# Kernel optimization log

Measured on AMD Instinct MI355X. Metric: run time of the kernel, lower is better.

## Reference

```python
import jax, jax.numpy as jnp
import numpy as np
from jax import lax

# --- static config (matches init_kwargs) ---
K_NAT, P_NAT, NHEAD, DM, L = 5, 2, 8, 128, 3
PK, OV, STRIDE = 4, 2, 2          # patcher kernel / overlap / stride = PK-OV
PPAD = PK - OV                    # circular pad for patcher/depatcher crop
RK, RC = 5, 12                    # res layer kernel, hidden channels = 3*4
DN = ('NCHW', 'OIHW', 'NCHW')


def setup_inputs() -> dict:
    key = jax.random.key(0)
    ks = jax.random.split(key, 16)
    B, C, H, W = 2, 3, 256, 256
    rn = lambda k, shape, s=0.02: jax.random.normal(k, shape, jnp.float32) * s
    return {
        'x': jax.random.normal(ks[0], (B, C, H, W), jnp.float32),
        'pos_w': jax.random.uniform(ks[1], (C, H, W), jnp.float32) + 0.5,
        'pos_b': jax.random.uniform(ks[2], (C, H, W), jnp.float32) - 0.5,
        'patch_w': rn(ks[3], (DM, C, PK, PK), 0.05),
        'patch_b': jnp.zeros((DM,), jnp.float32),
        'ln1_g': jnp.ones((L, DM), jnp.float32),
        'ln1_b': jnp.zeros((L, DM), jnp.float32),
        'qkv_w': rn(ks[4], (L, 3 * DM, DM)),
        'qkv_b': jnp.zeros((L, 3 * DM), jnp.float32),
        'rpb': rn(ks[5], (L, NHEAD, 2 * K_NAT - 1, 2 * K_NAT - 1)),
        'proj_w': rn(ks[6], (L, DM, DM)),
        'proj_b': jnp.zeros((L, DM), jnp.float32),
        'ln2_g': jnp.ones((L, DM), jnp.float32),
        'ln2_b': jnp.zeros((L, DM), jnp.float32),
        'fc1_w': rn(ks[7], (L, 4 * DM, DM)),
        'fc1_b': jnp.zeros((L, 4 * DM), jnp.float32),
        'fc2_w': rn(ks[8], (L, DM, 4 * DM)),
        'fc2_b': jnp.zeros((L, DM), jnp.float32),
        'depatch_w': rn(ks[9], (DM, C, PK, PK), 0.05),   # ConvTranspose2d weight (Cin,Cout,kh,kw)
        'depatch_b': jnp.zeros((C,), jnp.float32),
        'res_cv1_w': rn(ks[10], (RC, C, RK, RK), 0.05),
        'res_cv1_b': jnp.zeros((RC,), jnp.float32),
        'res_cv2_w': rn(ks[11], (C, RC, 1, 1), 0.05),
        'res_cv2_b': jnp.zeros((C,), jnp.float32),
    }


def _layer_norm(x, g, b):
    m = x.mean(-1, keepdims=True)
    v = x.var(-1, keepdims=True)
    return (x - m) * lax.rsqrt(v + 1e-5) * g + b


def _nat_block(x, ln1_g, ln1_b, qkv_w, qkv_b, rpb, proj_w, proj_b,
               ln2_g, ln2_b, fc1_w, fc1_b, fc2_w, fc2_b):
    # x: (B,H,W,C). NATLayer: LN -> circular pad by k//2 -> NA -> crop -> residual -> LN -> MLP -> residual.
    # After padding, every kept (interior) pixel has a full centered kxk neighborhood,
    # so we compute q only at interior positions and gather kxk K/V windows from the padded map.
    B, H, W, C = x.shape
    k, p, h = K_NAT, P_NAT, NHEAD
    dh = C // h
    y = _layer_norm(x, ln1_g, ln1_b)
    y = jnp.pad(y, ((0, 0), (p, p), (p, p), (0, 0)), mode='wrap')  # circular
    qkv = y @ qkv_w.T + qkv_b                                      # (B,H+2p,W+2p,3C)
    q, kk, vv = jnp.split(qkv, 3, axis=-1)
    q = q[:, p:p + H, p:p + W].reshape(B, H, W, h, dh) * (dh ** -0.5)
    def win(t):
        t = t.reshape(B, H + 2 * p, W + 2 * p, h, dh)
        return jnp.stack([t[:, i:i + H, j:j + W]
                          for i in range(k) for j in range(k)], axis=3)  # (B,H,W,k*k,h,dh)
    kw, vw = win(kk), win(vv)
    bias = rpb[:, p:p + k, p:p + k].reshape(h, k * k)  # centered slice of (2k-1,2k-1) RPB
    logits = jnp.einsum('bxyhd,bxynhd->bxyhn', q, kw) + bias
    a = jax.nn.softmax(logits, axis=-1)
    o = jnp.einsum('bxyhn,bxynhd->bxyhd', a, vw).reshape(B, H, W, C)
    x = x + (o @ proj_w.T + proj_b)
    y = _layer_norm(x, ln2_g, ln2_b)
    y = jax.nn.leaky_relu(y @ fc1_w.T + fc1_b) @ fc2_w.T + fc2_b
    return x + y


def _forward(x, pos_w, pos_b, patch_w, patch_b, ln1_g, ln1_b, qkv_w, qkv_b,
             rpb, proj_w, proj_b, ln2_g, ln2_b, fc1_w, fc1_b, fc2_w, fc2_b,
             depatch_w, depatch_b, res_cv1_w, res_cv1_b, res_cv2_w, res_cv2_b):
    # positional embedding (dropout is identity, p=0)
    x = x * pos_w + pos_b
    # OverlapConvPatcher: circular pad by (PK-OV), conv kernel PK stride PK-OV -> (B,129,129,DM)
    xp = jnp.pad(x, ((0, 0), (0, 0), (PPAD, PPAD), (PPAD, PPAD)), mode='wrap')
    f = lax.conv_general_dilated(xp, patch_w, (STRIDE, STRIDE), 'VALID',
                                 dimension_numbers=DN) + patch_b[None, :, None, None]
    f = f.transpose(0, 2, 3, 1)
    for i in range(L):
        f = _nat_block(f, ln1_g[i], ln1_b[i], qkv_w[i], qkv_b[i], rpb[i],
                       proj_w[i], proj_b[i], ln2_g[i], ln2_b[i],
                       fc1_w[i], fc1_b[i], fc2_w[i], fc2_b[i])
    # OverlapDeconvDepatcher: ConvTranspose2d (kernel PK, stride PK-OV), crop PPAD border
    f = f.transpose(0, 3, 1, 2)
    wf = jnp.flip(depatch_w, (2, 3)).transpose(1, 0, 2, 3)  # (Cout,Cin,kh,kw)
    y = lax.conv_general_dilated(f, wf, (1, 1), [(PK - 1, PK - 1)] * 2,
                                 lhs_dilation=(STRIDE, STRIDE),
                                 dimension_numbers=DN) + depatch_b[None, :, None, None]
    y = y[:, :, PPAD:-PPAD, PPAD:-PPAD]  # (B,3,256,256)
    # ResLayer: circular-pad same conv 5x5 -> leaky_relu -> 1x1 conv -> residual
    yp = jnp.pad(y, ((0, 0), (0, 0), (RK // 2, RK // 2), (RK // 2, RK // 2)), mode='wrap')
    r = lax.conv_general_dilated(yp, res_cv1_w, (1, 1), 'VALID',
                                 dimension_numbers=DN) + res_cv1_b[None, :, None, None]
    r = jax.nn.leaky_relu(r)
    r = lax.conv_general_dilated(r, res_cv2_w, (1, 1), 'VALID',
                                 dimension_numbers=DN) + res_cv2_b[None, :, None, None]
    return y + r


def reference(x, pos_w, pos_b, patch_w, patch_b, ln1_g, ln1_b, qkv_w, qkv_b,
              rpb, proj_w, proj_b, ln2_g, ln2_b, fc1_w, fc1_b, fc2_w, fc2_b,
              depatch_w, depatch_b, res_cv1_w, res_cv1_b, res_cv2_w, res_cv2_b):
    return _forward(x, pos_w, pos_b, patch_w, patch_b, ln1_g, ln1_b, qkv_w, qkv_b,
                    rpb, proj_w, proj_b, ln2_g, ln2_b, fc1_w, fc1_b, fc2_w, fc2_b,
                    depatch_w, depatch_b, res_cv1_w, res_cv1_b, res_cv2_w, res_cv2_b)
```

## Files before the change

kernel.cpp:

```cpp
#include <hip/hip_runtime.h>
#include <hip/hip_bf16.h>
#include <math.h>

#define HF 129
#define WF 129
#define BDIM 2
#define TOK (BDIM*HF*WF)
#define DMOD 128

typedef __attribute__((ext_vector_type(8))) short short8;
typedef __attribute__((ext_vector_type(8))) unsigned short ushort8;
typedef __attribute__((ext_vector_type(4))) float f32x4;

__device__ __forceinline__ float leaky(float v){ return v > 0.f ? v : 0.01f*v; }
__device__ __forceinline__ float bf2f(unsigned short u){ return __uint_as_float(((unsigned int)u) << 16); }
__device__ __forceinline__ unsigned short f2bf(float f){
    unsigned int u = __float_as_uint(f);
    unsigned int r = (u + 0x7fff + ((u >> 16) & 1)) >> 16;
    return (unsigned short)r;
}

#define NQ 147456
#define NPJ 49152
#define N1 196608
#define N2 196608
#define NPAT 8192
#define NDEP 8192
__global__ __launch_bounds__(256) void prep_weights(
    const float* __restrict__ qkv_w, const float* __restrict__ proj_w,
    const float* __restrict__ fc1_w, const float* __restrict__ fc2_w,
    const float* __restrict__ patch_w, const float* __restrict__ dep_w,
    __hip_bfloat16* __restrict__ wq, __hip_bfloat16* __restrict__ wp,
    __hip_bfloat16* __restrict__ w1, __hip_bfloat16* __restrict__ w2,
    __hip_bfloat16* __restrict__ wpat, __hip_bfloat16* __restrict__ wdep,
    float* __restrict__ zero64)
{
    int off = blockIdx.x*256 + threadIdx.x;
    if (off < NQ) { wq[off] = __float2bfloat16(qkv_w[off]); return; } off -= NQ;
    if (off < NPJ){ wp[off] = __float2bfloat16(proj_w[off]); return; } off -= NPJ;
    if (off < N1) { w1[off] = __float2bfloat16(fc1_w[off]); return; } off -= N1;
    if (off < N2) { w2[off] = __float2bfloat16(fc2_w[off]); return; } off -= N2;
    if (off < NPAT){ int r = off>>6, e = off&63;
        wpat[off] = __float2bfloat16(e < 48 ? patch_w[r*48 + e] : 0.f); return; } off -= NPAT;
    if (off < NDEP){ int e = off>>7, d = off&127;
        wdep[off] = __float2bfloat16(e < 48 ? dep_w[d*48 + e] : 0.f); return; } off -= NDEP;
    if (off < 64) zero64[off] = 0.f;
}

__global__ __launch_bounds__(256) void im2col_kernel(
    const float* __restrict__ x, const float* __restrict__ pos_w, const float* __restrict__ pos_b,
    __hip_bfloat16* __restrict__ G)
{
    __shared__ float xs[12][260];
    int blk = blockIdx.x;
    int b = blk / HF, oh = blk - b*HF;
    int tid = threadIdx.x;
    #pragma unroll
    for (int it = 0; it < 3; ++it) {
        int p = it*4 + (tid >> 6);
        int c = p >> 2, r = p & 3;
        int h = (oh*2 + r - 2 + 256) & 255;
        int w4 = (tid & 63) * 4;
        float4 xv  = *(const float4*)(x     + ((size_t)(b*3 + c)*256 + h)*256 + w4);
        float4 pwv = *(const float4*)(pos_w + ((size_t)c*256 + h)*256 + w4);
        float4 pbv = *(const float4*)(pos_b + ((size_t)c*256 + h)*256 + w4);
        float4 o; o.x = xv.x*pwv.x + pbv.x; o.y = xv.y*pwv.y + pbv.y;
        o.z = xv.z*pwv.z + pbv.z; o.w = xv.w*pwv.w + pbv.w;
        *(float4*)&xs[p][w4] = o;
    }
    __syncthreads();
    int e = tid & 63, og = tid >> 6;
    int c = e >> 4, k = e & 15, kh = k >> 2, kw = k & 3;
    int p = c*4 + kh;
    unsigned short* Grow = (unsigned short*)G + (size_t)blk*WF*64;
    for (int ow = og; ow < WF; ow += 4) {
        unsigned short v = 0;
        if (e < 48) {
            int col = (ow*2 + kw - 2 + 256) & 255;
            v = f2bf(xs[p][col]);
        }
        Grow[ow*64 + e] = v;
    }
}

template<int ACT, int RES, int OUTF, int LNE>
__global__ __launch_bounds__(256) void gemmF_kernel(
    const __hip_bfloat16* __restrict__ A, const __hip_bfloat16* __restrict__ W,
    const float* __restrict__ bias, const float* __restrict__ lng, const float* __restrict__ lnb,
    __hip_bfloat16* __restrict__ Cbf, float* __restrict__ Cf,
    __hip_bfloat16* __restrict__ yl, int M, int N, int K)
{
    __shared__ __align__(16) char As[64*128];
    __shared__ __align__(16) char Ws[128*128];
    __shared__ float2 lnred[64][2];
    int tid = threadIdx.x;
    int bm = blockIdx.x*64, bn = blockIdx.y*128;
    int lane = tid & 63, wid = tid >> 6;
    int wr = (wid >> 1)*32, wc = (wid & 1)*64;
    int lrow = lane & 15, lq = lane >> 4;
    int srow = tid >> 3, scg = tid & 7;
    int swz = (lrow & 7) << 4;
    int awo0 = ((srow     )*128 + scg*16) ^ ((srow&7)<<4);
    int awo1 = ((srow + 32)*128 + scg*16) ^ ((srow&7)<<4);

    bool v0 = (bm + srow) < M, v1 = (bm + srow + 32) < M;
    const __hip_bfloat16* a0p = A + (size_t)(bm + srow)*K + scg*8;
    const __hip_bfloat16* a1p = A + (size_t)(bm + srow + 32)*K + scg*8;
    const __hip_bfloat16* wp0 = W + (size_t)(bn + srow)*K + scg*8;

    f32x4 acc[2][4] = {};
    for (int k0 = 0; k0 < K; k0 += 64) {
        int4 va0 = {}, va1 = {};
        if (v0) va0 = *(const int4*)(a0p + k0);
        if (v1) va1 = *(const int4*)(a1p + k0);
        int4 vw0 = *(const int4*)(wp0 + k0);
        int4 vw1 = *(const int4*)(wp0 + (size_t)32*K + k0);
        int4 vw2 = *(const int4*)(wp0 + (size_t)64*K + k0);
        int4 vw3 = *(const int4*)(wp0 + (size_t)96*K + k0);
        __syncthreads();
        *(int4*)(As + awo0) = va0;
        *(int4*)(As + awo1) = va1;
        *(int4*)(Ws + awo0) = vw0;
        *(int4*)(Ws + awo1) = vw1;
        *(int4*)(Ws + (((srow+64)*128 + scg*16) ^ ((srow&7)<<4))) = vw2;
        *(int4*)(Ws + (((srow+96)*128 + scg*16) ^ ((srow&7)<<4))) = vw3;
        __syncthreads();
        #pragma unroll
        for (int ks = 0; ks < 2; ++ks) {
            int kb = ks*64;
            short8 af[2], bf[4];
            #pragma unroll
            for (int mi = 0; mi < 2; ++mi)
                af[mi] = *(const short8*)(As + (((wr + mi*16 + lrow)*128 + kb + lq*16) ^ swz));
            #pragma unroll
            for (int ni = 0; ni < 4; ++ni)
                bf[ni] = *(const short8*)(Ws + (((wc + ni*16 + lrow)*128 + kb + lq*16) ^ swz));
            #pragma unroll
            for (int mi = 0; mi < 2; ++mi)
                #pragma unroll
                for (int ni = 0; ni < 4; ++ni)
                    acc[mi][ni] = __builtin_amdgcn_mfma_f32_16x16x32_bf16(af[mi], bf[ni], acc[mi][ni], 0, 0, 0);
        }
    }
    float bcol[4];
    #pragma unroll
    for (int ni = 0; ni < 4; ++ni) bcol[ni] = bias[bn + wc + ni*16 + lrow];
    #pragma unroll
    for (int mi = 0; mi < 2; ++mi) {
        #pragma unroll
        for (int r = 0; r < 4; ++r) {
            int row = bm + wr + mi*16 + lq*4 + r;
            bool vrow = row < M;
            #pragma unroll
            for (int ni = 0; ni < 4; ++ni) {
                float v = acc[mi][ni][r] + bcol[ni];
                if (ACT) v = leaky(v);
                if (RES || OUTF) {
                    int col = wc + ni*16 + lrow;
                    size_t idx = (size_t)row*128 + col;
                    if (RES) { float old = vrow ? Cf[idx] : 0.f; v += old; }
                    if (vrow) Cf[idx] = v;
                } else {
                    int col = bn + wc + ni*16 + lrow;
                    if (vrow) Cbf[(size_t)row*N + col] = __float2bfloat16(v);
                }
                acc[mi][ni][r] = v;
            }
        }
    }
    if (LNE) {
        float sa[8], ssa[8];
        #pragma unroll
        for (int mi = 0; mi < 2; ++mi)
            #pragma unroll
            for (int r = 0; r < 4; ++r) {
                float s = 0.f, ss = 0.f;
                #pragma unroll
                for (int ni = 0; ni < 4; ++ni) { float v = acc[mi][ni][r]; s += v; ss += v*v; }
                sa[mi*4+r] = s; ssa[mi*4+r] = ss;
            }
        #pragma unroll
        for (int m = 1; m < 16; m <<= 1) {
            #pragma unroll
            for (int i = 0; i < 8; ++i) { sa[i] += __shfl_xor(sa[i], m); ssa[i] += __shfl_xor(ssa[i], m); }
        }
        if (lrow == 0) {
            #pragma unroll
            for (int i = 0; i < 8; ++i)
                lnred[wr + (i>>2)*16 + lq*4 + (i&3)][wc>>6] = make_float2(sa[i], ssa[i]);
        }
        __syncthreads();
        float gcol[4], bbcol[4];
        #pragma unroll
        for (int ni = 0; ni < 4; ++ni) {
            gcol[ni] = lng[wc + ni*16 + lrow];
            bbcol[ni] = lnb[wc + ni*16 + lrow];
        }
        #pragma unroll
        for (int mi = 0; mi < 2; ++mi) {
            #pragma unroll
            for (int r = 0; r < 4; ++r) {
                int rl = wr + mi*16 + lq*4 + r;
                int row = bm + rl;
                if (row >= M) continue;
                float2 h0 = lnred[rl][0], h1 = lnred[rl][1];
                float mean = (h0.x + h1.x) * (1.f/128.f);
                float var = (h0.y + h1.y) * (1.f/128.f) - mean*mean;
                float inv = rsqrtf(var + 1e-5f);
                #pragma unroll
                for (int ni = 0; ni < 4; ++ni) {
                    int col = wc + ni*16 + lrow;
                    float yv = (acc[mi][ni][r] - mean)*inv*gcol[ni] + bbcol[ni];
                    yl[(size_t)row*128 + col] = __float2bfloat16(yv);
                }
            }
        }
    }
}

template<int ACT, int RES, int OUTF, int A32>
__global__ __launch_bounds__(256) void mgemm_kernel(
    const void* __restrict__ Av, const __hip_bfloat16* __restrict__ W,
    const float* __restrict__ bias, __hip_bfloat16* __restrict__ Cbf,
    float* __restrict__ Cres, int M, int N, int K)
{
    __shared__ __align__(16) char As[64*128];
    __shared__ __align__(16) char Ws[64*128];
    int tid = threadIdx.x;
    int bm = blockIdx.x*64, bn = blockIdx.y*64;
    int lane = tid & 63, wid = tid >> 6;
    int wm = (wid >> 1)*32, wn = (wid & 1)*32;
    int lrow = lane & 15, lq = lane >> 4;
    int srow = tid >> 3, scg = tid & 7;
    int wo0 = ((srow     )*128 + scg*16) ^ ((srow&7)<<4);
    int wo1 = ((srow + 32)*128 + scg*16) ^ ((srow&7)<<4);
    int swz = (lrow & 7) << 4;
    int baseA0 = (wm + lrow     )*128 + lq*16;
    int baseA1 = (wm + 16 + lrow)*128 + lq*16;
    int baseB0 = (wn + lrow     )*128 + lq*16;
    int baseB1 = (wn + 16 + lrow)*128 + lq*16;

    f32x4 acc[2][2] = {};
    bool v0 = (bm + srow) < M, v1 = (bm + srow + 32) < M;
    const __hip_bfloat16* a0p = (const __hip_bfloat16*)Av + (size_t)(bm + srow)*K + scg*8;
    const __hip_bfloat16* a1p = (const __hip_bfloat16*)Av + (size_t)(bm + srow + 32)*K + scg*8;
    const float* a0pf = (const float*)Av + (size_t)(bm + srow)*K + scg*8;
    const float* a1pf = (const float*)Av + (size_t)(bm + srow + 32)*K + scg*8;
    const __hip_bfloat16* w0p = W + (size_t)(bn + srow)*K + scg*8;
    const __hip_bfloat16* w1p = W + (size_t)(bn + srow + 32)*K + scg*8;

    for (int k0 = 0; k0 < K; k0 += 64) {
        int4 va0 = {}, va1 = {};
        if (A32) {
            if (v0) {
                float4 p0 = *(const float4*)(a0pf + k0);
                float4 p1 = *(const float4*)(a0pf + k0 + 4);
                va0.x = f2bf(p0.x) | (f2bf(p0.y) << 16); va0.y = f2bf(p0.z) | (f2bf(p0.w) << 16);
                va0.z = f2bf(p1.x) | (f2bf(p1.y) << 16); va0.w = f2bf(p1.z) | (f2bf(p1.w) << 16);
            }
            if (v1) {
                float4 p0 = *(const float4*)(a1pf + k0);
                float4 p1 = *(const float4*)(a1pf + k0 + 4);
                va1.x = f2bf(p0.x) | (f2bf(p0.y) << 16); va1.y = f2bf(p0.z) | (f2bf(p0.w) << 16);
                va1.z = f2bf(p1.x) | (f2bf(p1.y) << 16); va1.w = f2bf(p1.z) | (f2bf(p1.w) << 16);
            }
        } else {
            if (v0) va0 = *(const int4*)(a0p + k0);
            if (v1) va1 = *(const int4*)(a1p + k0);
        }
        int4 vw0 = *(const int4*)(w0p + k0);
        int4 vw1 = *(const int4*)(w1p + k0);
        __syncthreads();
        *(int4*)(As + wo0) = va0;
        *(int4*)(As + wo1) = va1;
        *(int4*)(Ws + wo0) = vw0;
        *(int4*)(Ws + wo1) = vw1;
        __syncthreads();
        #pragma unroll
        for (int ks = 0; ks < 2; ++ks) {
            int kb = ks*64;
            short8 a0 = *(const short8*)(As + ((baseA0 + kb) ^ swz));
            short8 a1 = *(const short8*)(As + ((baseA1 + kb) ^ swz));
            short8 b0 = *(const short8*)(Ws + ((baseB0 + kb) ^ swz));
            short8 b1 = *(const short8*)(Ws + ((baseB1 + kb) ^ swz));
            acc[0][0] = __builtin_amdgcn_mfma_f32_16x16x32_bf16(a0, b0, acc[0][0], 0, 0, 0);
            acc[0][1] = __builtin_amdgcn_mfma_f32_16x16x32_bf16(a0, b1, acc[0][1], 0, 0, 0);
            acc[1][0] = __builtin_amdgcn_mfma_f32_16x16x32_bf16(a1, b0, acc[1][0], 0, 0, 0);
            acc[1][1] = __builtin_amdgcn_mfma_f32_16x16x32_bf16(a1, b1, acc[1][1], 0, 0, 0);
        }
    }
    float bv0 = bias[bn + wn + lrow];
    float bv1 = bias[bn + wn + 16 + lrow];
    #pragma unroll
    for (int mi = 0; mi < 2; ++mi) {
        #pragma unroll
        for (int r = 0; r < 4; ++r) {
            int row = bm + wm + mi*16 + lq*4 + r;
            if (row >= M) continue;
            #pragma unroll
            for (int ni = 0; ni < 2; ++ni) {
                float v = acc[mi][ni][r] + (ni ? bv1 : bv0);
                if (ACT == 1) v = leaky(v);
                int col = bn + wn + ni*16 + lrow;
                if (RES)       Cres[(size_t)row*N + col] += v;
                else if (OUTF) Cres[(size_t)row*N + col] = v;
                else           Cbf[(size_t)row*N + col] = __float2bfloat16(v);
            }
        }
    }
}

__global__ __launch_bounds__(256) void attn_kernel(const __hip_bfloat16* __restrict__ qkv,
    const float* __restrict__ rpb, __hip_bfloat16* __restrict__ o)
{
    int gid = blockIdx.x*256 + threadIdx.x;
    int tok = gid >> 3;
    if (tok >= TOK) return;
    int head = gid & 7;
    int b = tok / (HF*WF);
    int rem = tok - b*HF*WF;
    int y = rem / WF, x = rem - y*WF;
    const ushort8* qp = (const ushort8*)(qkv + (size_t)tok*384 + head*16);
    float q[16];
    {
        ushort8 u0 = qp[0], u1 = qp[1];
        #pragma unroll
        for (int i = 0; i < 8; ++i) { q[i] = bf2f(u0[i])*0.25f; q[i+8] = bf2f(u1[i])*0.25f; }
    }
    float logits[25];
    float mx = -1e30f;
    #pragma unroll
    for (int di = -2; di <= 2; ++di) {
        int ny = y + di; ny += (ny < 0) ? HF : 0; ny -= (ny >= HF) ? HF : 0;
        #pragma unroll
        for (int dj = -2; dj <= 2; ++dj) {
            int nx = x + dj; nx += (nx < 0) ? WF : 0; nx -= (nx >= WF) ? WF : 0;
            size_t nt = (size_t)((b*HF + ny)*WF + nx);
            const ushort8* kp = (const ushort8*)(qkv + nt*384 + 128 + head*16);
            ushort8 k0 = kp[0], k1 = kp[1];
            float d = 0.f;
            #pragma unroll
            for (int i = 0; i < 8; ++i) d += q[i]*bf2f(k0[i]) + q[i+8]*bf2f(k1[i]);
            d += rpb[head*81 + (di+4)*9 + (dj+4)];
            logits[(di+2)*5 + (dj+2)] = d;
            mx = fmaxf(mx, d);
        }
    }
    float s = 0.f;
    #pragma unroll
    for (int n = 0; n < 25; ++n) { float p = __expf(logits[n]-mx); logits[n] = p; s += p; }
    float invs = 1.f/s;
    float outv[16] = {};
    #pragma unroll
    for (int di = -2; di <= 2; ++di) {
        int ny = y + di; ny += (ny < 0) ? HF : 0; ny -= (ny >= HF) ? HF : 0;
        #pragma unroll
        for (int dj = -2; dj <= 2; ++dj) {
            int nx = x + dj; nx += (nx < 0) ? WF : 0; nx -= (nx >= WF) ? WF : 0;
            size_t nt = (size_t)((b*HF + ny)*WF + nx);
            const ushort8* vp = (const ushort8*)(qkv + nt*384 + 256 + head*16);
            ushort8 v0 = vp[0], v1 = vp[1];
            float p = logits[(di+2)*5 + (dj+2)];
            #pragma unroll
            for (int i = 0; i < 8; ++i) { outv[i] += p*bf2f(v0[i]); outv[i+8] += p*bf2f(v1[i]); }
        }
    }
    __hip_bfloat16* op = o + (size_t)tok*DMOD + head*16;
    #pragma unroll
    for (int i = 0; i < 16; ++i) op[i] = __float2bfloat16(outv[i]*invs);
}

__global__ __launch_bounds__(256) void degather_kernel(const float* __restrict__ G,
    const float* __restrict__ db, float* __restrict__ yimg)
{
    int idx = blockIdx.x*256 + threadIdx.x;
    int b = idx >> 16;
    int pix = idx & 65535;
    int i = pix >> 8, j = pix & 255;
    int fh0 = i >> 1, fw0 = j >> 1;
    size_t r00 = ((size_t)(b*HF + fh0)*WF + fw0)*64;
    size_t r01 = r00 + 64;
    size_t r10 = r00 + (size_t)WF*64;
    size_t r11 = r10 + 64;
    int wr0 = (2 + (i & 1))*4, wr1 = (i & 1)*4;
    int wc0 = 2 + (j & 1), wc1 = (j & 1);
    #pragma unroll
    for (int c = 0; c < 3; ++c) {
        int e = c*16;
        float v = db[c]
                + G[r00 + e + wr0 + wc0] + G[r01 + e + wr0 + wc1]
                + G[r10 + e + wr1 + wc0] + G[r11 + e + wr1 + wc1];
        yimg[((size_t)(b*3 + c) << 16) + pix] = v;
    }
}

__global__ __launch_bounds__(256) void res_kernel(const float* __restrict__ y,
    const float* __restrict__ w1, const float* __restrict__ b1,
    const float* __restrict__ w2, const float* __restrict__ b2, float* __restrict__ out)
{
    int idx = blockIdx.x*256 + threadIdx.x;
    int b = idx >> 16;
    int pix = idx & 65535;
    int i = pix >> 8, j = pix & 255;
    float yv[3][5][5];
    #pragma unroll
    for (int c = 0; c < 3; ++c) {
        #pragma unroll
        for (int u = 0; u < 5; ++u) {
            int ii = (i + u - 2 + 256) & 255;
            #pragma unroll
            for (int v = 0; v < 5; ++v) {
                int jj = (j + v - 2 + 256) & 255;
                yv[c][u][v] = y[((size_t)(b*3 + c)*256 + ii)*256 + jj];
            }
        }
    }
    float r1[12];
    #pragma unroll
    for (int rc = 0; rc < 12; ++rc) {
        float a = b1[rc];
        #pragma unroll
        for (int c = 0; c < 3; ++c)
            #pragma unroll
            for (int u = 0; u < 5; ++u)
                #pragma unroll
                for (int v = 0; v < 5; ++v)
                    a += yv[c][u][v] * w1[rc*75 + c*25 + u*5 + v];
        r1[rc] = leaky(a);
    }
    #pragma unroll
    for (int c = 0; c < 3; ++c) {
        float a = b2[c];
        #pragma unroll
        for (int rc = 0; rc < 12; ++rc) a += r1[rc]*w2[c*12 + rc];
        out[((size_t)(b*3 + c)*256 + i)*256 + j] = yv[c][2][2] + a;
    }
}

extern "C" void kernel_launch(void* const* d_in, const int* in_sizes, int n_in,
                              void* d_out, int out_size, void* d_ws, size_t ws_size,
                              hipStream_t stream)
{
    const float* x      = (const float*)d_in[0];
    const float* pos_w  = (const float*)d_in[1];
    const float* pos_b  = (const float*)d_in[2];
    const float* patch_w= (const float*)d_in[3];
    const float* patch_b= (const float*)d_in[4];
    const float* ln1_g  = (const float*)d_in[5];
    const float* ln1_b  = (const float*)d_in[6];
    const float* qkv_w  = (const float*)d_in[7];
    const float* qkv_b  = (const float*)d_in[8];
    const float* rpb    = (const float*)d_in[9];
    const float* proj_w = (const float*)d_in[10];
    const float* proj_b = (const float*)d_in[11];
    const float* ln2_g  = (const float*)d_in[12];
    const float* ln2_b  = (const float*)d_in[13];
    const float* fc1_w  = (const float*)d_in[14];
    const float* fc1_b  = (const float*)d_in[15];
    const float* fc2_w  = (const float*)d_in[16];
    const float* fc2_b  = (const float*)d_in[17];
    const float* dep_w  = (const float*)d_in[18];
    const float* dep_b  = (const float*)d_in[19];
    const float* rc1_w  = (const float*)d_in[20];
    const float* rc1_b  = (const float*)d_in[21];
    const float* rc2_w  = (const float*)d_in[22];
    const float* rc2_b  = (const float*)d_in[23];

    const size_t SZ = (size_t)TOK * 128;
    char* w = (char*)d_ws;
    float* f            = (float*)w;            w += SZ*4;
    __hip_bfloat16* yln = (__hip_bfloat16*)w;   w += SZ*2;
    __hip_bfloat16* ao  = (__hip_bfloat16*)w;   w += SZ*2;
    __hip_bfloat16* qkvb= (__hip_bfloat16*)w;   w += (size_t)TOK*384*2;
    __hip_bfloat16* hb  = (__hip_bfloat16*)w;   w += (size_t)TOK*512*2;
    float* yimg         = (float*)w;            w += (size_t)BDIM*3*65536*4;
    __hip_bfloat16* wq  = (__hip_bfloat16*)w;   w += (size_t)NQ*2;
    __hip_bfloat16* wp  = (__hip_bfloat16*)w;   w += (size_t)NPJ*2;
    __hip_bfloat16* w1  = (__hip_bfloat16*)w;   w += (size_t)N1*2;
    __hip_bfloat16* w2  = (__hip_bfloat16*)w;   w += (size_t)N2*2;
    __hip_bfloat16* wpat= (__hip_bfloat16*)w;   w += (size_t)NPAT*2;
    __hip_bfloat16* wdep= (__hip_bfloat16*)w;   w += (size_t)NDEP*2;
    float* zero64       = (float*)w;            w += 64*4;

    __hip_bfloat16* icol = qkvb;
    float* G             = (float*)hb;

    const int PREP_TOT = NQ + NPJ + N1 + N2 + NPAT + NDEP + 64;
    prep_weights<<<(PREP_TOT + 255)/256, 256, 0, stream>>>(
        qkv_w, proj_w, fc1_w, fc2_w, patch_w, dep_w, wq, wp, w1, w2, wpat, wdep, zero64);

    im2col_kernel<<<BDIM*HF, 256, 0, stream>>>(x, pos_w, pos_b, icol);

    const int GM = (TOK + 63)/64;

    gemmF_kernel<0,0,1,1><<<dim3(GM,1), 256, 0, stream>>>(icol, wpat, patch_b,
        ln1_g, ln1_b, nullptr, f, yln, TOK, 128, 64);

    for (int l = 0; l < 3; ++l) {
        gemmF_kernel<0,0,0,0><<<dim3(GM,3), 256, 0, stream>>>(yln, wq + (size_t)l*384*128,
            qkv_b + l*384, nullptr, nullptr, qkvb, nullptr, nullptr, TOK, 384, 128);
        attn_kernel<<<(TOK*8 + 255)/256, 256, 0, stream>>>(qkvb, rpb + l*8*81, ao);
        gemmF_kernel<0,1,0,1><<<dim3(GM,1), 256, 0, stream>>>(ao, wp + (size_t)l*128*128,
            proj_b + l*128, ln2_g + l*128, ln2_b + l*128, nullptr, f, yln, TOK, 128, 128);
        gemmF_kernel<1,0,0,0><<<dim3(GM,4), 256, 0, stream>>>(yln, w1 + (size_t)l*512*128,
            fc1_b + l*512, nullptr, nullptr, hb, nullptr, nullptr, TOK, 512, 128);
        if (l < 2)
            gemmF_kernel<0,1,0,1><<<dim3(GM,1), 256, 0, stream>>>(hb, w2 + (size_t)l*128*512,
                fc2_b + l*128, ln1_g + (l+1)*128, ln1_b + (l+1)*128, nullptr, f, yln, TOK, 128, 512);
        else
            gemmF_kernel<0,1,0,0><<<dim3(GM,1), 256, 0, stream>>>(hb, w2 + (size_t)l*128*512,
                fc2_b + l*128, nullptr, nullptr, nullptr, f, nullptr, TOK, 128, 512);
    }

    mgemm_kernel<0,0,1,1><<<dim3(GM,1), 256, 0, stream>>>(f, wdep, zero64,
        nullptr, G, TOK, 64, 128);
    degather_kernel<<<512, 256, 0, stream>>>(G, dep_b, yimg);

    res_kernel<<<512, 256, 0, stream>>>(yimg, rc1_w, rc1_b, rc2_w, rc2_b, (float*)d_out);
}
```

Measured before the change: 361.3 us.

## Fuse MLP fc1 and fc2 into one kernel keeping hidden activations in LDS

Replaces the separate fc1 GEMM (which wrote a TOK x 512 bf16 hidden buffer to global memory) and the fc2 GEMM with a single mlp_kernel. Each block handles 32 tokens, computes the 512-wide leaky-ReLU hidden tile into shared memory, then runs fc2 plus residual and the optional LayerNorm epilogue. This removes the global round trip for the hidden activations and one launch per layer. In exchange each block reloads the full W1 and W2 weights for only 32 rows, and LDS use is about 72KB per block, which can limit occupancy.

```diff
diff --git a/kernel.cpp b/kernel.cpp
--- a/kernel.cpp
+++ b/kernel.cpp
@@ -14,10 +14,9 @@
 
 __device__ __forceinline__ float leaky(float v){ return v > 0.f ? v : 0.01f*v; }
 __device__ __forceinline__ float bf2f(unsigned short u){ return __uint_as_float(((unsigned int)u) << 16); }
-__device__ __forceinline__ unsigned short f2bf(float f){
+__device__ __forceinline__ unsigned int f2bf(float f){
     unsigned int u = __float_as_uint(f);
-    unsigned int r = (u + 0x7fff + ((u >> 16) & 1)) >> 16;
-    return (unsigned short)r;
+    return (u + 0x7fff + ((u >> 16) & 1)) >> 16;
 }
 
 #define NQ 147456
@@ -77,7 +76,7 @@
         unsigned short v = 0;
         if (e < 48) {
             int col = (ow*2 + kw - 2 + 256) & 255;
-            v = f2bf(xs[p][col]);
+            v = (unsigned short)f2bf(xs[p][col]);
         }
         Grow[ow*64 + e] = v;
     }
@@ -211,6 +210,192 @@
                 for (int ni = 0; ni < 4; ++ni) {
                     int col = wc + ni*16 + lrow;
                     float yv = (acc[mi][ni][r] - mean)*inv*gcol[ni] + bbcol[ni];
+                    yl[(size_t)row*128 + col] = __float2bfloat16(yv);
+                }
+            }
+        }
+    }
+}
+
+template<int LNE>
+__global__ __launch_bounds__(256) void mlp_kernel(
+    const __hip_bfloat16* __restrict__ A, const __hip_bfloat16* __restrict__ W1,
+    const float* __restrict__ b1, const __hip_bfloat16* __restrict__ W2,
+    const float* __restrict__ b2, const float* __restrict__ lng, const float* __restrict__ lnb,
+    float* __restrict__ f, __hip_bfloat16* __restrict__ yl, int M)
+{
+    __shared__ __align__(16) char Ain[2*32*128];
+    __shared__ __align__(16) char Wb[2*128*128];
+    __shared__ __align__(16) char Hb[8*32*128];
+    __shared__ float2 lnred[32][4];
+    int tid = threadIdx.x;
+    int bm = blockIdx.x*32;
+    int lane = tid & 63, wid = tid >> 6;
+    int wc = wid*32;
+    int lrow = lane & 15, lq = lane >> 4;
+    int srow = tid >> 3, scg = tid & 7;
+    int swz = (lrow & 7) << 4;
+    int sswz = (srow & 7) << 4;
+
+    bool vr = (bm + srow) < M;
+    {
+        const __hip_bfloat16* ap = A + (size_t)(bm + srow)*128 + scg*8;
+        int4 z = {0,0,0,0};
+        #pragma unroll
+        for (int p = 0; p < 2; ++p) {
+            int4 v = vr ? *(const int4*)(ap + p*64) : z;
+            *(int4*)(Ain + p*4096 + srow*128 + (scg*16 ^ sswz)) = v;
+        }
+    }
+
+    for (int c = 0; c < 4; ++c) {
+        if (c) __syncthreads();
+        #pragma unroll
+        for (int rr = 0; rr < 4; ++rr) {
+            int row = rr*32 + srow;
+            const __hip_bfloat16* wp = W1 + (size_t)(c*128 + row)*128 + scg*8;
+            int rswz = (row & 7) << 4;
+            #pragma unroll
+            for (int p = 0; p < 2; ++p) {
+                int4 v = *(const int4*)(wp + p*64);
+                *(int4*)(Wb + p*16384 + row*128 + (scg*16 ^ rswz)) = v;
+            }
+        }
+        __syncthreads();
+        f32x4 acc1[2][2] = {};
+        #pragma unroll
+        for (int ks = 0; ks < 4; ++ks) {
+            int p = ks >> 1, kb = (ks & 1)*64 + lq*16;
+            short8 af[2], bfr[2];
+            #pragma unroll
+            for (int mi = 0; mi < 2; ++mi)
+                af[mi] = *(const short8*)(Wb + p*16384 + (wc + mi*16 + lrow)*128 + (kb ^ swz));
+            #pragma unroll
+            for (int ni = 0; ni < 2; ++ni)
+                bfr[ni] = *(const short8*)(Ain + p*4096 + (ni*16 + lrow)*128 + (kb ^ swz));
+            #pragma unroll
+            for (int mi = 0; mi < 2; ++mi)
+                #pragma unroll
+                for (int ni = 0; ni < 2; ++ni)
+                    acc1[mi][ni] = __builtin_amdgcn_mfma_f32_16x16x32_bf16(af[mi], bfr[ni], acc1[mi][ni], 0, 0, 0);
+        }
+        #pragma unroll
+        for (int mi = 0; mi < 2; ++mi) {
+            float4 bv = *(const float4*)(b1 + c*128 + wc + mi*16 + lq*4);
+            #pragma unroll
+            for (int ni = 0; ni < 2; ++ni) {
+                float u0 = leaky(acc1[mi][ni][0] + bv.x);
+                float u1 = leaky(acc1[mi][ni][1] + bv.y);
+                float u2 = leaky(acc1[mi][ni][2] + bv.z);
+                float u3 = leaky(acc1[mi][ni][3] + bv.w);
+                int2 pk;
+                pk.x = (int)(f2bf(u0) | (f2bf(u1) << 16));
+                pk.y = (int)(f2bf(u2) | (f2bf(u3) << 16));
+                int t = ni*16 + lrow;
+                int hh = c*128 + wc + mi*16 + lq*4;
+                int byteo = (hh >> 6)*4096 + t*128 + ((((hh & 63)*2)) ^ ((t & 7) << 4));
+                *(int2*)(Hb + byteo) = pk;
+            }
+        }
+    }
+
+    f32x4 acc2[2][2] = {};
+    for (int kc = 0; kc < 4; ++kc) {
+        __syncthreads();
+        #pragma unroll
+        for (int rr = 0; rr < 4; ++rr) {
+            int row = rr*32 + srow;
+            const __hip_bfloat16* wp = W2 + (size_t)row*512 + kc*128 + scg*8;
+            int rswz = (row & 7) << 4;
+            #pragma unroll
+            for (int p = 0; p < 2; ++p) {
+                int4 v = *(const int4*)(wp + p*64);
+                *(int4*)(Wb + p*16384 + row*128 + (scg*16 ^ rswz)) = v;
+            }
+        }
+        __syncthreads();
+        #pragma unroll
+        for (int ks = 0; ks < 4; ++ks) {
+            int p = ks >> 1, kb = (ks & 1)*64 + lq*16;
+            short8 af[2], bfr[2];
+            #pragma unroll
+            for (int mi = 0; mi < 2; ++mi)
+                af[mi] = *(const short8*)(Hb + (kc*2 + p)*4096 + (mi*16 + lrow)*128 + (kb ^ swz));
+            #pragma unroll
+            for (int ni = 0; ni < 2; ++ni)
+                bfr[ni] = *(const short8*)(Wb + p*16384 + (wc + ni*16 + lrow)*128 + (kb ^ swz));
+            #pragma unroll
+            for (int mi = 0; mi < 2; ++mi)
+                #pragma unroll
+                for (int ni = 0; ni < 2; ++ni)
+                    acc2[mi][ni] = __builtin_amdgcn_mfma_f32_16x16x32_bf16(af[mi], bfr[ni], acc2[mi][ni], 0, 0, 0);
+        }
+    }
+    float bcol[2];
+    #pragma unroll
+    for (int ni = 0; ni < 2; ++ni) bcol[ni] = b2[wc + ni*16 + lrow];
+    #pragma unroll
+    for (int mi = 0; mi < 2; ++mi) {
+        #pragma unroll
+        for (int r = 0; r < 4; ++r) {
+            int row = bm + mi*16 + lq*4 + r;
+            bool vrow = row < M;
+            #pragma unroll
+            for (int ni = 0; ni < 2; ++ni) {
+                int col = wc + ni*16 + lrow;
+                size_t idx = (size_t)row*128 + col;
+                float v = acc2[mi][ni][r] + bcol[ni];
+                float old = vrow ? f[idx] : 0.f;
+                v += old;
+                if (vrow) f[idx] = v;
+                acc2[mi][ni][r] = v;
+            }
+        }
+    }
+    if (LNE) {
+        float sa[8], ssa[8];
+        #pragma unroll
+        for (int mi = 0; mi < 2; ++mi)
+            #pragma unroll
+            for (int r = 0; r < 4; ++r) {
+                float s = 0.f, ss = 0.f;
+                #pragma unroll
+                for (int ni = 0; ni < 2; ++ni) { float v = acc2[mi][ni][r]; s += v; ss += v*v; }
+                sa[mi*4+r] = s; ssa[mi*4+r] = ss;
+            }
+        #pragma unroll
+        for (int m = 1; m < 16; m <<= 1) {
+            #pragma unroll
+            for (int i = 0; i < 8; ++i) { sa[i] += __shfl_xor(sa[i], m); ssa[i] += __shfl_xor(ssa[i], m); }
+        }
+        if (lrow == 0) {
+            #pragma unroll
+            for (int i = 0; i < 8; ++i)
+                lnred[(i>>2)*16 + lq*4 + (i&3)][wid] = make_float2(sa[i], ssa[i]);
+        }
+        __syncthreads();
+        float gcol[2], bbcol[2];
+        #pragma unroll
+        for (int ni = 0; ni < 2; ++ni) {
+            gcol[ni] = lng[wc + ni*16 + lrow];
+            bbcol[ni] = lnb[wc + ni*16 + lrow];
+        }
+        #pragma unroll
+        for (int mi = 0; mi < 2; ++mi) {
+            #pragma unroll
+            for (int r = 0; r < 4; ++r) {
+                int rl = mi*16 + lq*4 + r;
+                int row = bm + rl;
+                if (row >= M) continue;
+                float2 h0 = lnred[rl][0], h1 = lnred[rl][1];
+                float2 h2 = lnred[rl][2], h3 = lnred[rl][3];
+                float mean = (h0.x + h1.x + h2.x + h3.x) * (1.f/128.f);
+                float var = (h0.y + h1.y + h2.y + h3.y) * (1.f/128.f) - mean*mean;
+                float inv = rsqrtf(var + 1e-5f);
+                #pragma unroll
+                for (int ni = 0; ni < 2; ++ni) {
+                    int col = wc + ni*16 + lrow;
+                    float yv = (acc2[mi][ni][r] - mean)*inv*gcol[ni] + bbcol[ni];
                     yl[(size_t)row*128 + col] = __float2bfloat16(yv);
                 }
             }
@@ -255,14 +440,14 @@
             if (v0) {
                 float4 p0 = *(const float4*)(a0pf + k0);
                 float4 p1 = *(const float4*)(a0pf + k0 + 4);
-                va0.x = f2bf(p0.x) | (f2bf(p0.y) << 16); va0.y = f2bf(p0.z) | (f2bf(p0.w) << 16);
-                va0.z = f2bf(p1.x) | (f2bf(p1.y) << 16); va0.w = f2bf(p1.z) | (f2bf(p1.w) << 16);
+                va0.x = (int)(f2bf(p0.x) | (f2bf(p0.y) << 16)); va0.y = (int)(f2bf(p0.z) | (f2bf(p0.w) << 16));
+                va0.z = (int)(f2bf(p1.x) | (f2bf(p1.y) << 16)); va0.w = (int)(f2bf(p1.z) | (f2bf(p1.w) << 16));
             }
             if (v1) {
                 float4 p0 = *(const float4*)(a1pf + k0);
                 float4 p1 = *(const float4*)(a1pf + k0 + 4);
-                va1.x = f2bf(p0.x) | (f2bf(p0.y) << 16); va1.y = f2bf(p0.z) | (f2bf(p0.w) << 16);
-                va1.z = f2bf(p1.x) | (f2bf(p1.y) << 16); va1.w = f2bf(p1.z) | (f2bf(p1.w) << 16);
+                va1.x = (int)(f2bf(p0.x) | (f2bf(p0.y) << 16)); va1.y = (int)(f2bf(p0.z) | (f2bf(p0.w) << 16));
+                va1.z = (int)(f2bf(p1.x) | (f2bf(p1.y) << 16)); va1.w = (int)(f2bf(p1.z) | (f2bf(p1.w) << 16));
             }
         } else {
             if (v0) va0 = *(const int4*)(a0p + k0);
@@ -492,6 +677,7 @@
     im2col_kernel<<<BDIM*HF, 256, 0, stream>>>(x, pos_w, pos_b, icol);
 
     const int GM = (TOK + 63)/64;
+    const int GM32 = (TOK + 31)/32;
 
     gemmF_kernel<0,0,1,1><<<dim3(GM,1), 256, 0, stream>>>(icol, wpat, patch_b,
         ln1_g, ln1_b, nullptr, f, yln, TOK, 128, 64);
@@ -502,14 +688,14 @@
         attn_kernel<<<(TOK*8 + 255)/256, 256, 0, stream>>>(qkvb, rpb + l*8*81, ao);
         gemmF_kernel<0,1,0,1><<<dim3(GM,1), 256, 0, stream>>>(ao, wp + (size_t)l*128*128,
             proj_b + l*128, ln2_g + l*128, ln2_b + l*128, nullptr, f, yln, TOK, 128, 128);
-        gemmF_kernel<1,0,0,0><<<dim3(GM,4), 256, 0, stream>>>(yln, w1 + (size_t)l*512*128,
-            fc1_b + l*512, nullptr, nullptr, hb, nullptr, nullptr, TOK, 512, 128);
         if (l < 2)
-            gemmF_kernel<0,1,0,1><<<dim3(GM,1), 256, 0, stream>>>(hb, w2 + (size_t)l*128*512,
-                fc2_b + l*128, ln1_g + (l+1)*128, ln1_b + (l+1)*128, nullptr, f, yln, TOK, 128, 512);
+            mlp_kernel<1><<<GM32, 256, 0, stream>>>(yln, w1 + (size_t)l*512*128, fc1_b + l*512,
+                w2 + (size_t)l*128*512, fc2_b + l*128,
+                ln1_g + (l+1)*128, ln1_b + (l+1)*128, f, yln, TOK);
         else
-            gemmF_kernel<0,1,0,0><<<dim3(GM,1), 256, 0, stream>>>(hb, w2 + (size_t)l*128*512,
-                fc2_b + l*128, nullptr, nullptr, nullptr, f, nullptr, TOK, 128, 512);
+            mlp_kernel<0><<<GM32, 256, 0, stream>>>(yln, w1 + (size_t)l*512*128, fc1_b + l*512,
+                w2 + (size_t)l*128*512, fc2_b + l*128,
+                nullptr, nullptr, f, nullptr, TOK);
     }
 
     mgemm_kernel<0,0,1,1><<<dim3(GM,1), 256, 0, stream>>>(f, wdep, zero64,
```

Measured after the change: 377.5 us. 4.5% more time.

## Fuse neighborhood attention, proj GEMM+LN2, and FC1 GEMM into one kernel

Applied to the files above, without the earlier changes.

Replaces the separate attention, proj+residual+LN2, and FC1 kernels with one kernel per 32-token tile. Attention output is written straight into swizzled LDS and fed to the proj MFMA. The LayerNorm result stays in LDS as the A operand for four FC1 column chunks. This removes the global round-trips of the attention output and the LN2 activations, plus two launches per layer. In exchange, the 32-row tiles cut MFMA reuse, and weights are reloaded per block with no overlap between loads and compute.

```diff
diff --git a/kernel.cpp b/kernel.cpp
--- a/kernel.cpp
+++ b/kernel.cpp
@@ -14,10 +14,9 @@
 
 __device__ __forceinline__ float leaky(float v){ return v > 0.f ? v : 0.01f*v; }
 __device__ __forceinline__ float bf2f(unsigned short u){ return __uint_as_float(((unsigned int)u) << 16); }
-__device__ __forceinline__ unsigned short f2bf(float f){
+__device__ __forceinline__ unsigned int f2bf(float f){
     unsigned int u = __float_as_uint(f);
-    unsigned int r = (u + 0x7fff + ((u >> 16) & 1)) >> 16;
-    return (unsigned short)r;
+    return (u + 0x7fff + ((u >> 16) & 1)) >> 16;
 }
 
 #define NQ 147456
@@ -77,7 +76,7 @@
         unsigned short v = 0;
         if (e < 48) {
             int col = (ow*2 + kw - 2 + 256) & 255;
-            v = f2bf(xs[p][col]);
+            v = (unsigned short)f2bf(xs[p][col]);
         }
         Grow[ow*64 + e] = v;
     }
@@ -218,6 +217,200 @@
     }
 }
 
+__global__ __launch_bounds__(256) void apf_kernel(
+    const __hip_bfloat16* __restrict__ qkv, const float* __restrict__ rpb,
+    const __hip_bfloat16* __restrict__ Wp, const float* __restrict__ pb,
+    const float* __restrict__ lng, const float* __restrict__ lnb,
+    const __hip_bfloat16* __restrict__ W1, const float* __restrict__ b1f,
+    float* __restrict__ f, __hip_bfloat16* __restrict__ hb, int M)
+{
+    __shared__ __align__(16) char As0[32*128];
+    __shared__ __align__(16) char As1[32*128];
+    __shared__ __align__(16) char Ws[128*128];
+    __shared__ float2 lnred[32][2];
+    int tid = threadIdx.x;
+    int bm = blockIdx.x*32;
+    int lane = tid & 63, wid = tid >> 6;
+    int wr = (wid >> 1)*16, wc = (wid & 1)*64;
+    int lrow = lane & 15, lq = lane >> 4;
+    int srow = tid >> 3, scg = tid & 7;
+    int swz = (lrow & 7) << 4;
+
+    {
+        int tloc = tid >> 3, head = tid & 7;
+        int tok = bm + tloc; if (tok >= M) tok = M - 1;
+        int b = tok / (HF*WF);
+        int rem = tok - b*HF*WF;
+        int y = rem / WF, x = rem - y*WF;
+        const ushort8* qp = (const ushort8*)(qkv + (size_t)tok*384 + head*16);
+        float q[16];
+        {
+            ushort8 u0 = qp[0], u1 = qp[1];
+            #pragma unroll
+            for (int i = 0; i < 8; ++i) { q[i] = bf2f(u0[i])*0.25f; q[i+8] = bf2f(u1[i])*0.25f; }
+        }
+        float logits[25];
+        float mx = -1e30f;
+        #pragma unroll
+        for (int di = -2; di <= 2; ++di) {
+            int ny = y + di; ny += (ny < 0) ? HF : 0; ny -= (ny >= HF) ? HF : 0;
+            #pragma unroll
+            for (int dj = -2; dj <= 2; ++dj) {
+                int nx = x + dj; nx += (nx < 0) ? WF : 0; nx -= (nx >= WF) ? WF : 0;
+                size_t nt = (size_t)((b*HF + ny)*WF + nx);
+                const ushort8* kp = (const ushort8*)(qkv + nt*384 + 128 + head*16);
+                ushort8 k0v = kp[0], k1v = kp[1];
+                float d = 0.f;
+                #pragma unroll
+                for (int i = 0; i < 8; ++i) d += q[i]*bf2f(k0v[i]) + q[i+8]*bf2f(k1v[i]);
+                d += rpb[head*81 + (di+4)*9 + (dj+4)];
+                logits[(di+2)*5 + (dj+2)] = d;
+                mx = fmaxf(mx, d);
+            }
+        }
+        float s = 0.f;
+        #pragma unroll
+        for (int n = 0; n < 25; ++n) { float p = __expf(logits[n]-mx); logits[n] = p; s += p; }
+        float invs = 1.f/s;
+        float outv[16] = {};
+        #pragma unroll
+        for (int di = -2; di <= 2; ++di) {
+            int ny = y + di; ny += (ny < 0) ? HF : 0; ny -= (ny >= HF) ? HF : 0;
+            #pragma unroll
+            for (int dj = -2; dj <= 2; ++dj) {
+                int nx = x + dj; nx += (nx < 0) ? WF : 0; nx -= (nx >= WF) ? WF : 0;
+                size_t nt = (size_t)((b*HF + ny)*WF + nx);
+                const ushort8* vp = (const ushort8*)(qkv + nt*384 + 256 + head*16);
+                ushort8 v0 = vp[0], v1 = vp[1];
+                float p = logits[(di+2)*5 + (dj+2)];
+                #pragma unroll
+                for (int i = 0; i < 8; ++i) { outv[i] += p*bf2f(v0[i]); outv[i+8] += p*bf2f(v1[i]); }
+            }
+        }
+        unsigned int pk[8];
+        #pragma unroll
+        for (int i = 0; i < 8; ++i)
+            pk[i] = f2bf(outv[2*i]*invs) | (f2bf(outv[2*i+1]*invs) << 16);
+        char* dst = (head < 4) ? As0 : As1;
+        int ro = tloc*128 + (head & 3)*32;
+        int sw = (tloc & 7) << 4;
+        int4 wv0; wv0.x = (int)pk[0]; wv0.y = (int)pk[1]; wv0.z = (int)pk[2]; wv0.w = (int)pk[3];
+        int4 wv1; wv1.x = (int)pk[4]; wv1.y = (int)pk[5]; wv1.z = (int)pk[6]; wv1.w = (int)pk[7];
+        *(int4*)(dst + (ro ^ sw)) = wv0;
+        *(int4*)(dst + ((ro + 16) ^ sw)) = wv1;
+    }
+
+    f32x4 acc[4] = {};
+    #pragma unroll
+    for (int k0 = 0; k0 < 128; k0 += 64) {
+        __syncthreads();
+        #pragma unroll
+        for (int rr = 0; rr < 4; ++rr) {
+            int row = rr*32 + srow;
+            int4 v = *(const int4*)(Wp + (size_t)row*128 + k0 + scg*8);
+            *(int4*)(Ws + row*128 + ((scg*16) ^ ((row&7)<<4))) = v;
+        }
+        __syncthreads();
+        const char* Ah = k0 ? As1 : As0;
+        #pragma unroll
+        for (int ks = 0; ks < 2; ++ks) {
+            int kb = ks*64 + lq*16;
+            short8 a = *(const short8*)(Ah + (((wr + lrow)*128 + kb) ^ swz));
+            #pragma unroll
+            for (int ni = 0; ni < 4; ++ni) {
+                short8 bfr = *(const short8*)(Ws + (((wc + ni*16 + lrow)*128 + kb) ^ swz));
+                acc[ni] = __builtin_amdgcn_mfma_f32_16x16x32_bf16(a, bfr, acc[ni], 0, 0, 0);
+            }
+        }
+    }
+    float sa[4] = {}, ssa[4] = {};
+    #pragma unroll
+    for (int ni = 0; ni < 4; ++ni) {
+        float bv = pb[wc + ni*16 + lrow];
+        #pragma unroll
+        for (int r = 0; r < 4; ++r) {
+            int rl = wr + lq*4 + r;
+            int row = bm + rl;
+            float v = acc[ni][r] + bv;
+            size_t idx = (size_t)row*128 + wc + ni*16 + lrow;
+            if (row < M) { v += f[idx]; f[idx] = v; }
+            acc[ni][r] = v;
+            sa[r] += v; ssa[r] += v*v;
+        }
+    }
+    #pragma unroll
+    for (int m = 1; m < 16; m <<= 1) {
+        #pragma unroll
+        for (int r = 0; r < 4; ++r) { sa[r] += __shfl_xor(sa[r], m); ssa[r] += __shfl_xor(ssa[r], m); }
+    }
+    if (lrow == 0) {
+        #pragma unroll
+        for (int r = 0; r < 4; ++r) lnred[wr + lq*4 + r][wc>>6] = make_float2(sa[r], ssa[r]);
+    }
+    __syncthreads();
+    {
+        float gc[4], bc2[4];
+        #pragma unroll
+        for (int ni = 0; ni < 4; ++ni) {
+            gc[ni]  = lng[wc + ni*16 + lrow];
+            bc2[ni] = lnb[wc + ni*16 + lrow];
+        }
+        char* half = wc ? As1 : As0;
+        #pragma unroll
+        for (int r = 0; r < 4; ++r) {
+            int rl = wr + lq*4 + r;
+            float2 h0 = lnred[rl][0], h1 = lnred[rl][1];
+            float mean = (h0.x + h1.x) * (1.f/128.f);
+            float inv = rsqrtf((h0.y + h1.y) * (1.f/128.f) - mean*mean + 1e-5f);
+            #pragma unroll
+            for (int ni = 0; ni < 4; ++ni) {
+                float yv = (acc[ni][r] - mean)*inv*gc[ni] + bc2[ni];
+                int co = ni*16 + lrow;
+                *(unsigned short*)(half + ((rl*128 + co*2) ^ ((rl&7)<<4))) = (unsigned short)f2bf(yv);
+            }
+        }
+    }
+
+    for (int c = 0; c < 4; ++c) {
+        f32x4 acc1[4] = {};
+        #pragma unroll
+        for (int k0 = 0; k0 < 128; k0 += 64) {
+            __syncthreads();
+            #pragma unroll
+            for (int rr = 0; rr < 4; ++rr) {
+                int row = rr*32 + srow;
+                int4 v = *(const int4*)(W1 + (size_t)(c*128 + row)*128 + k0 + scg*8);
+                *(int4*)(Ws + row*128 + ((scg*16) ^ ((row&7)<<4))) = v;
+            }
+            __syncthreads();
+            const char* Ah = k0 ? As1 : As0;
+            #pragma unroll
+            for (int ks = 0; ks < 2; ++ks) {
+                int kb = ks*64 + lq*16;
+                short8 a = *(const short8*)(Ah + (((wr + lrow)*128 + kb) ^ swz));
+                #pragma unroll
+                for (int ni = 0; ni < 4; ++ni) {
+                    short8 bfr = *(const short8*)(Ws + (((wc + ni*16 + lrow)*128 + kb) ^ swz));
+                    acc1[ni] = __builtin_amdgcn_mfma_f32_16x16x32_bf16(a, bfr, acc1[ni], 0, 0, 0);
+                }
+            }
+        }
+        #pragma unroll
+        for (int ni = 0; ni < 4; ++ni) {
+            int col = c*128 + wc + ni*16 + lrow;
+            float bv = b1f[col];
+            #pragma unroll
+            for (int r = 0; r < 4; ++r) {
+                int row = bm + wr + lq*4 + r;
+                if (row < M) {
+                    float v = leaky(acc1[ni][r] + bv);
+                    hb[(size_t)row*512 + col] = __float2bfloat16(v);
+                }
+            }
+        }
+    }
+}
+
 template<int ACT, int RES, int OUTF, int A32>
 __global__ __launch_bounds__(256) void mgemm_kernel(
     const void* __restrict__ Av, const __hip_bfloat16* __restrict__ W,
@@ -255,14 +448,14 @@
             if (v0) {
                 float4 p0 = *(const float4*)(a0pf + k0);
                 float4 p1 = *(const float4*)(a0pf + k0 + 4);
-                va0.x = f2bf(p0.x) | (f2bf(p0.y) << 16); va0.y = f2bf(p0.z) | (f2bf(p0.w) << 16);
-                va0.z = f2bf(p1.x) | (f2bf(p1.y) << 16); va0.w = f2bf(p1.z) | (f2bf(p1.w) << 16);
+                va0.x = (int)(f2bf(p0.x) | (f2bf(p0.y) << 16)); va0.y = (int)(f2bf(p0.z) | (f2bf(p0.w) << 16));
+                va0.z = (int)(f2bf(p1.x) | (f2bf(p1.y) << 16)); va0.w = (int)(f2bf(p1.z) | (f2bf(p1.w) << 16));
             }
             if (v1) {
                 float4 p0 = *(const float4*)(a1pf + k0);
                 float4 p1 = *(const float4*)(a1pf + k0 + 4);
-                va1.x = f2bf(p0.x) | (f2bf(p0.y) << 16); va1.y = f2bf(p0.z) | (f2bf(p0.w) << 16);
-                va1.z = f2bf(p1.x) | (f2bf(p1.y) << 16); va1.w = f2bf(p1.z) | (f2bf(p1.w) << 16);
+                va1.x = (int)(f2bf(p0.x) | (f2bf(p0.y) << 16)); va1.y = (int)(f2bf(p0.z) | (f2bf(p0.w) << 16));
+                va1.z = (int)(f2bf(p1.x) | (f2bf(p1.y) << 16)); va1.w = (int)(f2bf(p1.z) | (f2bf(p1.w) << 16));
             }
         } else {
             if (v0) va0 = *(const int4*)(a0p + k0);
@@ -308,66 +501,6 @@
             }
         }
     }
-}
-
-__global__ __launch_bounds__(256) void attn_kernel(const __hip_bfloat16* __restrict__ qkv,
-    const float* __restrict__ rpb, __hip_bfloat16* __restrict__ o)
-{
-    int gid = blockIdx.x*256 + threadIdx.x;
-    int tok = gid >> 3;
-    if (tok >= TOK) return;
-    int head = gid & 7;
-    int b = tok / (HF*WF);
-    int rem = tok - b*HF*WF;
-    int y = rem / WF, x = rem - y*WF;
-    const ushort8* qp = (const ushort8*)(qkv + (size_t)tok*384 + head*16);
-    float q[16];
-    {
-        ushort8 u0 = qp[0], u1 = qp[1];
-        #pragma unroll
-        for (int i = 0; i < 8; ++i) { q[i] = bf2f(u0[i])*0.25f; q[i+8] = bf2f(u1[i])*0.25f; }
-    }
-    float logits[25];
-    float mx = -1e30f;
-    #pragma unroll
-    for (int di = -2; di <= 2; ++di) {
-        int ny = y + di; ny += (ny < 0) ? HF : 0; ny -= (ny >= HF) ? HF : 0;
-        #pragma unroll
-        for (int dj = -2; dj <= 2; ++dj) {
-            int nx = x + dj; nx += (nx < 0) ? WF : 0; nx -= (nx >= WF) ? WF : 0;
-            size_t nt = (size_t)((b*HF + ny)*WF + nx);
-            const ushort8* kp = (const ushort8*)(qkv + nt*384 + 128 + head*16);
-            ushort8 k0 = kp[0], k1 = kp[1];
-            float d = 0.f;
-            #pragma unroll
-            for (int i = 0; i < 8; ++i) d += q[i]*bf2f(k0[i]) + q[i+8]*bf2f(k1[i]);
-            d += rpb[head*81 + (di+4)*9 + (dj+4)];
-            logits[(di+2)*5 + (dj+2)] = d;
-            mx = fmaxf(mx, d);
-        }
-    }
-    float s = 0.f;
-    #pragma unroll
-    for (int n = 0; n < 25; ++n) { float p = __expf(logits[n]-mx); logits[n] = p; s += p; }
-    float invs = 1.f/s;
-    float outv[16] = {};
-    #pragma unroll
-    for (int di = -2; di <= 2; ++di) {
-        int ny = y + di; ny += (ny < 0) ? HF : 0; ny -= (ny >= HF) ? HF : 0;
-        #pragma unroll
-        for (int dj = -2; dj <= 2; ++dj) {
-            int nx = x + dj; nx += (nx < 0) ? WF : 0; nx -= (nx >= WF) ? WF : 0;
-            size_t nt = (size_t)((b*HF + ny)*WF + nx);
-            const ushort8* vp = (const ushort8*)(qkv + nt*384 + 256 + head*16);
-            ushort8 v0 = vp[0], v1 = vp[1];
-            float p = logits[(di+2)*5 + (dj+2)];
-            #pragma unroll
-            for (int i = 0; i < 8; ++i) { outv[i] += p*bf2f(v0[i]); outv[i+8] += p*bf2f(v1[i]); }
-        }
-    }
-    __hip_bfloat16* op = o + (size_t)tok*DMOD + head*16;
-    #pragma unroll
-    for (int i = 0; i < 16; ++i) op[i] = __float2bfloat16(outv[i]*invs);
 }
 
 __global__ __launch_bounds__(256) void degather_kernel(const float* __restrict__ G,
@@ -470,7 +603,6 @@
     char* w = (char*)d_ws;
     float* f            = (float*)w;            w += SZ*4;
     __hip_bfloat16* yln = (__hip_bfloat16*)w;   w += SZ*2;
-    __hip_bfloat16* ao  = (__hip_bfloat16*)w;   w += SZ*2;
     __hip_bfloat16* qkvb= (__hip_bfloat16*)w;   w += (size_t)TOK*384*2;
     __hip_bfloat16* hb  = (__hip_bfloat16*)w;   w += (size_t)TOK*512*2;
     float* yimg         = (float*)w;            w += (size_t)BDIM*3*65536*4;
@@ -492,6 +624,7 @@
     im2col_kernel<<<BDIM*HF, 256, 0, stream>>>(x, pos_w, pos_b, icol);
 
     const int GM = (TOK + 63)/64;
+    const int GM32 = (TOK + 31)/32;
 
     gemmF_kernel<0,0,1,1><<<dim3(GM,1), 256, 0, stream>>>(icol, wpat, patch_b,
         ln1_g, ln1_b, nullptr, f, yln, TOK, 128, 64);
@@ -499,11 +632,10 @@
     for (int l = 0; l < 3; ++l) {
         gemmF_kernel<0,0,0,0><<<dim3(GM,3), 256, 0, stream>>>(yln, wq + (size_t)l*384*128,
             qkv_b + l*384, nullptr, nullptr, qkvb, nullptr, nullptr, TOK, 384, 128);
-        attn_kernel<<<(TOK*8 + 255)/256, 256, 0, stream>>>(qkvb, rpb + l*8*81, ao);
-        gemmF_kernel<0,1,0,1><<<dim3(GM,1), 256, 0, stream>>>(ao, wp + (size_t)l*128*128,
-            proj_b + l*128, ln2_g + l*128, ln2_b + l*128, nullptr, f, yln, TOK, 128, 128);
-        gemmF_kernel<1,0,0,0><<<dim3(GM,4), 256, 0, stream>>>(yln, w1 + (size_t)l*512*128,
-            fc1_b + l*512, nullptr, nullptr, hb, nullptr, nullptr, TOK, 512, 128);
+        apf_kernel<<<GM32, 256, 0, stream>>>(qkvb, rpb + l*8*81,
+            wp + (size_t)l*128*128, proj_b + l*128,
+            ln2_g + l*128, ln2_b + l*128,
+            w1 + (size_t)l*512*128, fc1_b + l*512, f, hb, TOK);
         if (l < 2)
             gemmF_kernel<0,1,0,1><<<dim3(GM,1), 256, 0, stream>>>(hb, w2 + (size_t)l*128*512,
                 fc2_b + l*128, ln1_g + (l+1)*128, ln1_b + (l+1)*128, nullptr, f, yln, TOK, 128, 512);
```

Result: slower. 527.8 us (+46.1%).
